# Kernel tuning notes

Hardware: AMD Instinct MI355X
Metric: run time of the kernel (lower is better)

The kernel has to match this reference:

```python
import jax, jax.numpy as jnp
import numpy as np

N = 50000
E = 400000
IN_DIM = 128
HID = 128
OUT = 128
HEADS = 8
NEG_SLOPE = 0.2  # PyG GATConv default
BN_EPS = 1e-5


def _gat_conv(x, W, a_src, a_dst, b, src, dst, concat):
    """PyG GATConv (eval): self-loops added by caller. x:[N,F], W:[F,H*C], a_*:[H,C]."""
    H, C = a_src.shape
    xW = (x @ W).reshape(N, H, C)                       # [N,H,C]
    es = jnp.sum(xW * a_src[None], axis=-1)             # [N,H]
    ed = jnp.sum(xW * a_dst[None], axis=-1)             # [N,H]
    e = jax.nn.leaky_relu(es[src] + ed[dst], NEG_SLOPE) # [E,H]
    m = jax.ops.segment_max(e, dst, num_segments=N)     # softmax over incoming edges per dst
    ex = jnp.exp(e - m[dst])
    denom = jax.ops.segment_sum(ex, dst, num_segments=N)
    alpha = ex / denom[dst]                             # [E,H]
    out = jax.ops.segment_sum(xW[src] * alpha[:, :, None], dst, num_segments=N)  # [N,H,C]
    out = out.reshape(N, H * C) if concat else out.mean(axis=1)
    return out + b


def _bn_eval(h, g, be, rm, rv):
    return (h - rm) * jax.lax.rsqrt(rv + BN_EPS) * g + be


def setup_inputs() -> dict:
    key = jax.random.key(0)
    ks = jax.random.split(key, 20)
    C1 = HID // HEADS
    f32 = jnp.float32
    inp = {
        "x": jax.random.normal(ks[0], (N, IN_DIM), dtype=f32),
        "edge_index": jax.random.randint(ks[1], (2, E), 0, N, dtype=jnp.int64),
        # GAT layer 1 (in->hid, 8 heads, concat)
        "W1": jax.random.normal(ks[2], (IN_DIM, HEADS * C1), dtype=f32) * 0.05,
        "a_src1": jax.random.normal(ks[3], (HEADS, C1), dtype=f32) * 0.05,
        "a_dst1": jax.random.normal(ks[4], (HEADS, C1), dtype=f32) * 0.05,
        "b1": jnp.zeros((HEADS * C1,), dtype=f32),
        # GAT layer 2 (hid->hid, 8 heads, concat)
        "W2": jax.random.normal(ks[5], (HID, HEADS * C1), dtype=f32) * 0.05,
        "a_src2": jax.random.normal(ks[6], (HEADS, C1), dtype=f32) * 0.05,
        "a_dst2": jax.random.normal(ks[7], (HEADS, C1), dtype=f32) * 0.05,
        "b2": jnp.zeros((HEADS * C1,), dtype=f32),
        # GAT layer 3 (hid->out, 1 head, no concat)
        "W3": jax.random.normal(ks[8], (HID, OUT), dtype=f32) * 0.05,
        "a_src3": jax.random.normal(ks[9], (1, OUT), dtype=f32) * 0.05,
        "a_dst3": jax.random.normal(ks[10], (1, OUT), dtype=f32) * 0.05,
        "b3": jnp.zeros((OUT,), dtype=f32),
        # residual linears
        "R1w": jax.random.normal(ks[11], (IN_DIM, HID), dtype=f32) * 0.05,
        "R1b": jnp.zeros((HID,), dtype=f32),
        "R2w": jax.random.normal(ks[12], (HID, HID), dtype=f32) * 0.05,
        "R2b": jnp.zeros((HID,), dtype=f32),
        "R3w": jax.random.normal(ks[13], (HID, OUT), dtype=f32) * 0.05,
        "R3b": jnp.zeros((OUT,), dtype=f32),
        # batch norms (eval mode: running stats)
        "g1": jnp.ones((HID,), dtype=f32), "be1": jnp.zeros((HID,), dtype=f32),
        "rm1": jnp.zeros((HID,), dtype=f32), "rv1": jnp.ones((HID,), dtype=f32),
        "g2": jnp.ones((HID,), dtype=f32), "be2": jnp.zeros((HID,), dtype=f32),
        "rm2": jnp.zeros((HID,), dtype=f32), "rv2": jnp.ones((HID,), dtype=f32),
    }
    return inp


def reference(x, edge_index, W1, a_src1, a_dst1, b1, W2, a_src2, a_dst2, b2,
              W3, a_src3, a_dst3, b3, R1w, R1b, R2w, R2b, R3w, R3b,
              g1, be1, rm1, rv1, g2, be2, rm2, rv2):
    # PyG GATConv adds self-loops by default
    loops = jnp.arange(N, dtype=edge_index.dtype)
    src = jnp.concatenate([edge_index[0], loops])
    dst = jnp.concatenate([edge_index[1], loops])

    h = _gat_conv(x, W1, a_src1, a_dst1, b1, src, dst, concat=True) + (x @ R1w + R1b)
    h1 = jax.nn.relu(_bn_eval(h, g1, be1, rm1, rv1))  # dropout identity in eval

    h = _gat_conv(h1, W2, a_src2, a_dst2, b2, src, dst, concat=True) + (h1 @ R2w + R2b)
    h2 = jax.nn.relu(_bn_eval(h, g2, be2, rm2, rv2))

    out = _gat_conv(h2, W3, a_src3, a_dst3, b3, src, dst, concat=False) + (h2 @ R3w + R3b)
    return out
```

## Files before the change

### kernel.cpp

```cpp
#include <hip/hip_runtime.h>
#include <hip/hip_bf16.h>
#include <type_traits>

typedef __hip_bfloat16 bf16;
typedef __hip_bfloat162 bf162;
typedef short v8s __attribute__((ext_vector_type(8)));
typedef float v4f __attribute__((ext_vector_type(4)));

__device__ __forceinline__ float lrelu(float x) { return x > 0.f ? x : 0.2f * x; }
__device__ __forceinline__ float b2f(bf16 v) { return __bfloat162float(v); }

__global__ void k_count(const int* __restrict__ ei, int* __restrict__ cnt, int E) {
    int i = blockIdx.x * 256 + threadIdx.x;
    if (i < E) atomicAdd(&cnt[ei[E + i]], 1);
}

__global__ void k_scan1(const int* __restrict__ cnt, int* __restrict__ ofs,
                        int* __restrict__ bsum, int n) {
    __shared__ int sh[256];
    int t = threadIdx.x;
    int base = blockIdx.x * 1024 + t * 4;
    int v[4]; int s = 0;
#pragma unroll
    for (int i = 0; i < 4; ++i) { v[i] = (base + i < n) ? cnt[base + i] : 0; s += v[i]; }
    sh[t] = s; __syncthreads();
    for (int o = 1; o < 256; o <<= 1) {
        int x = 0; if (t >= o) x = sh[t - o];
        __syncthreads();
        sh[t] += x;
        __syncthreads();
    }
    int excl = sh[t] - s;
#pragma unroll
    for (int i = 0; i < 4; ++i) { if (base + i < n) ofs[base + i] = excl; excl += v[i]; }
    if (t == 255) bsum[blockIdx.x] = sh[255];
}

__global__ void k_scan2(const int* __restrict__ bsum, int* __restrict__ bpre, int nb) {
    int l = threadIdx.x;
    int v = (l < nb) ? bsum[l] : 0;
    int orig = v;
    for (int o = 1; o < 64; o <<= 1) {
        int x = __shfl_up(v, o);
        if (l >= o) v += x;
    }
    if (l < nb) bpre[l] = v - orig;
}

__global__ void k_scan3(int* __restrict__ ofs, int* __restrict__ cur,
                        const int* __restrict__ bpre, int n) {
    int i = blockIdx.x * 256 + threadIdx.x;
    if (i < n) { int v = ofs[i] + bpre[i >> 10]; ofs[i] = v; cur[i] = v; }
}

__global__ void k_fill(const int* __restrict__ ei, int* __restrict__ cur,
                       int* __restrict__ csr, int E) {
    int i = blockIdx.x * 256 + threadIdx.x;
    if (i < E) {
        int d = ei[E + i];
        int pos = atomicAdd(&cur[d], 1);
        csr[pos] = ei[i];
    }
}

__global__ void k_trans(const float* __restrict__ s0, const float* __restrict__ s1,
                        const float* __restrict__ s2, const float* __restrict__ s3,
                        const float* __restrict__ s4, const float* __restrict__ s5,
                        const float* __restrict__ as1, const float* __restrict__ ad1,
                        const float* __restrict__ as2, const float* __restrict__ ad2,
                        const float* __restrict__ as3, const float* __restrict__ ad3,
                        const float* b1, const float* R1b, const float* g1, const float* be1,
                        const float* rm1, const float* rv1,
                        const float* b2, const float* R2b, const float* g2, const float* be2,
                        const float* rm2, const float* rv2,
                        const float* b3, const float* R3b,
                        bf16* __restrict__ wt, float* __restrict__ prm) {
    int b = blockIdx.x;
    int t = threadIdx.x;
    if (b == 6) {
        int c = t;
        if (c < 128) {
            float s1v = g1[c] * rsqrtf(rv1[c] + 1e-5f);
            prm[c]       = b1[c] + R1b[c];
            prm[128 + c] = s1v;
            prm[256 + c] = be1[c] - rm1[c] * s1v;
            float s2v = g2[c] * rsqrtf(rv2[c] + 1e-5f);
            prm[384 + c] = b2[c] + R2b[c];
            prm[512 + c] = s2v;
            prm[640 + c] = be2[c] - rm2[c] * s2v;
            prm[768 + c] = b3[c] + R3b[c];
        }
        return;
    }
    const float* src;
    switch (b) {
        case 0: src = s0; break; case 1: src = s1; break; case 2: src = s2; break;
        case 3: src = s3; break; case 4: src = s4; break; default: src = s5; break;
    }
    bf16* dst = wt + (size_t)b * 18432;
    for (int i = t; i < 16384; i += 256) {
        int k = i >> 7, n = i & 127;
        dst[n * 128 + k] = __float2bfloat16(src[i]);
    }
    if ((b & 1) == 0) {
        int layer = b >> 1;
        if (layer < 2) {
            const float* asr = (layer == 0) ? as1 : as2;
            const float* ads = (layer == 0) ? ad1 : ad2;
            for (int i = t; i < 2048; i += 256) {
                int row = i >> 7, k = i & 127, h = row & 7;
                const float* av = (row < 8) ? asr : ads;
                float s = 0.f;
#pragma unroll
                for (int c = 0; c < 16; ++c) s += src[k * 128 + h * 16 + c] * av[h * 16 + c];
                dst[(128 + row) * 128 + k] = __float2bfloat16(s);
            }
        } else {
            for (int i = t; i < 2048; i += 256) {
                int row = i >> 7, k = i & 127;
                float s = 0.f;
                if (row == 0 || row == 8) {
                    const float* av = (row == 0) ? as3 : ad3;
                    for (int c = 0; c < 128; ++c) s += src[k * 128 + c] * av[c];
                }
                dst[(128 + row) * 128 + k] = __float2bfloat16(s);
            }
        }
    } else {
        for (int i = t; i < 2048; i += 256)
            dst[16384 + i] = __float2bfloat16(0.f);
    }
}

template <typename T>
__global__ void gemm_dual(const T* __restrict__ A,
                          const bf16* __restrict__ BT0, const bf16* __restrict__ BT1,
                          bf16* __restrict__ O0, bf16* __restrict__ O1,
                          float* __restrict__ es, float* __restrict__ ed,
                          int mode, int nrows) {
    __shared__ bf16 Ash[128 * 128];
    __shared__ bf16 Bsh[144 * 128];
    const bf16* BT = (blockIdx.y == 0) ? BT0 : BT1;
    bf16* O = (blockIdx.y == 0) ? O0 : O1;
    const int t = threadIdx.x;
    const int rowbase = blockIdx.x * 128;
    {
        const int r = t >> 1, hf = t & 1;
        int gr = rowbase + r; if (gr >= nrows) gr = nrows - 1;
        if constexpr (std::is_same<T, float>::value) {
            const float4* asrc = (const float4*)(A + (size_t)gr * 128 + hf * 64);
#pragma unroll
            for (int j = 0; j < 8; ++j) {
                float4 u = asrc[2 * j], w = asrc[2 * j + 1];
                union { bf16 h[8]; float4 f; } tmp;
                tmp.h[0] = __float2bfloat16(u.x); tmp.h[1] = __float2bfloat16(u.y);
                tmp.h[2] = __float2bfloat16(u.z); tmp.h[3] = __float2bfloat16(u.w);
                tmp.h[4] = __float2bfloat16(w.x); tmp.h[5] = __float2bfloat16(w.y);
                tmp.h[6] = __float2bfloat16(w.z); tmp.h[7] = __float2bfloat16(w.w);
                int c = hf * 8 + j, cp = c ^ (r & 7);
                *(float4*)(&Ash[r * 128 + cp * 8]) = tmp.f;
            }
        } else {
            const float4* asrc = (const float4*)(A + (size_t)gr * 128 + hf * 64);
#pragma unroll
            for (int j = 0; j < 8; ++j) {
                int c = hf * 8 + j, cp = c ^ (r & 7);
                *(float4*)(&Ash[r * 128 + cp * 8]) = asrc[j];
            }
        }
    }
    for (int s = t; s < 288; s += 256) {
        int r = s >> 1, hf = s & 1;
        const float4* bsrc = (const float4*)(BT + r * 128 + hf * 64);
#pragma unroll
        for (int j = 0; j < 8; ++j) {
            int c = hf * 8 + j, cp = c ^ (r & 7);
            *(float4*)(&Bsh[r * 128 + cp * 8]) = bsrc[j];
        }
    }
    __syncthreads();
    const int wave = t >> 6, lane = t & 63, quad = lane >> 4, l16 = lane & 15;
    v4f acc[2][9];
#pragma unroll
    for (int i = 0; i < 2; ++i)
#pragma unroll
        for (int j = 0; j < 9; ++j) acc[i][j] = (v4f){0.f, 0.f, 0.f, 0.f};
#pragma unroll
    for (int kit = 0; kit < 4; ++kit) {
        v8s afr[2], bfr[9];
#pragma unroll
        for (int rt = 0; rt < 2; ++rt) {
            int row = wave * 32 + rt * 16 + l16;
            int cp = (kit * 4 + quad) ^ (row & 7);
            afr[rt] = *(const v8s*)(&Ash[row * 128 + cp * 8]);
        }
#pragma unroll
        for (int ct = 0; ct < 9; ++ct) {
            int nn = ct * 16 + l16;
            int cp = (kit * 4 + quad) ^ (nn & 7);
            bfr[ct] = *(const v8s*)(&Bsh[nn * 128 + cp * 8]);
        }
#pragma unroll
        for (int rt = 0; rt < 2; ++rt)
#pragma unroll
            for (int ct = 0; ct < 9; ++ct)
                acc[rt][ct] = __builtin_amdgcn_mfma_f32_16x16x32_bf16(afr[rt], bfr[ct], acc[rt][ct], 0, 0, 0);
    }
#pragma unroll
    for (int rt = 0; rt < 2; ++rt)
#pragma unroll
        for (int ct = 0; ct < 8; ++ct)
#pragma unroll
            for (int r = 0; r < 4; ++r) {
                int gr = rowbase + wave * 32 + rt * 16 + quad * 4 + r;
                if (gr < nrows) O[(size_t)gr * 128 + ct * 16 + l16] = __float2bfloat16(acc[rt][ct][r]);
            }
    if (mode != 0 && blockIdx.y == 0) {
#pragma unroll
        for (int rt = 0; rt < 2; ++rt)
#pragma unroll
            for (int r = 0; r < 4; ++r) {
                int gr = rowbase + wave * 32 + rt * 16 + quad * 4 + r;
                if (gr < nrows) {
                    float v = acc[rt][8][r];
                    if (mode == 1) {
                        if (l16 < 8) es[(size_t)gr * 8 + l16] = v;
                        else         ed[(size_t)gr * 8 + (l16 - 8)] = v;
                    } else {
                        if (l16 == 0) es[gr] = v;
                        else if (l16 == 8) ed[gr] = v;
                    }
                }
            }
    }
}

__global__ void k_agg8(const bf16* __restrict__ xW, const float* __restrict__ es8,
                       const float* __restrict__ ed8,
                       const int* __restrict__ ofs, const int* __restrict__ cur,
                       const int* __restrict__ csr,
                       const bf16* __restrict__ rres, const float* __restrict__ prm,
                       bf16* __restrict__ hout, int n) {
    int wave = threadIdx.x >> 6, lane = threadIdx.x & 63;
    int node = blockIdx.x * 4 + wave;
    if (node >= n) return;
    const int g = lane >> 4, l16 = lane & 15;
    const int c0 = l16 * 8;
    const int hc = l16 >> 1;
    const int he = lane & 7;
    float edw = ed8[(size_t)node * 8 + he];
    float wselfh = __expf(lrelu(es8[(size_t)node * 8 + he] + edw));
    float acc[8]; float den = 0.f;
#pragma unroll
    for (int i = 0; i < 8; ++i) acc[i] = 0.f;
    {
        float ws = __shfl(wselfh, hc);
        if (g == 0) {
            v8s xv = *(const v8s*)(xW + (size_t)node * 128 + c0);
            const bf16* xb = (const bf16*)&xv;
            den = ws;
#pragma unroll
            for (int i = 0; i < 8; ++i) acc[i] = ws * b2f(xb[i]);
        }
    }
    int beg = ofs[node], end = cur[node];
    for (int base = beg; base < end; base += 64) {
        int m = end - base; if (m > 64) m = 64;
        int idx = (lane < m) ? csr[base + lane] : node;
        for (int sub = 0; sub * 8 < m; ++sub) {
            int e = sub * 8 + (lane >> 3);
            int sidx = __shfl(idx, e & 63);
            float esv = es8[(size_t)sidx * 8 + he];
            float w = (e < m) ? __expf(lrelu(esv + edw)) : 0.f;
#pragma unroll
            for (int jj = 0; jj < 2; ++jj) {
                int jo = jj * 4 + g;
                int j = sub * 8 + jo;
                int sv = __shfl(idx, j & 63);
                float wj = __shfl(w, jo * 8 + hc);
                v8s xv = *(const v8s*)(xW + (size_t)sv * 128 + c0);
                const bf16* xb = (const bf16*)&xv;
                den += wj;
#pragma unroll
                for (int i = 0; i < 8; ++i) acc[i] += wj * b2f(xb[i]);
            }
        }
    }
    den += __shfl_xor(den, 16); den += __shfl_xor(den, 32);
#pragma unroll
    for (int i = 0; i < 8; ++i) {
        acc[i] += __shfl_xor(acc[i], 16);
        acc[i] += __shfl_xor(acc[i], 32);
    }
    if (g == 0) {
        float inv = 1.f / den;
        v8s rv = *(const v8s*)(rres + (size_t)node * 128 + c0);
        const bf16* rb = (const bf16*)&rv;
        bf16 outv[8];
#pragma unroll
        for (int i = 0; i < 8; ++i) {
            int c = c0 + i;
            float v = acc[i] * inv + prm[c] + b2f(rb[i]);
            v = fmaxf(v * prm[128 + c] + prm[256 + c], 0.f);
            outv[i] = __float2bfloat16(v);
        }
        *(v8s*)(hout + (size_t)node * 128 + c0) = *(v8s*)outv;
    }
}

__global__ void k_agg1(const bf16* __restrict__ xW, const float* __restrict__ es,
                       const float* __restrict__ ed,
                       const int* __restrict__ ofs, const int* __restrict__ cur,
                       const int* __restrict__ csr,
                       const bf16* __restrict__ rres, const float* __restrict__ bias,
                       float* __restrict__ out, int n) {
    int wave = threadIdx.x >> 6, lane = threadIdx.x & 63;
    int node = blockIdx.x * 4 + wave;
    if (node >= n) return;
    const int g = lane >> 4, l16 = lane & 15;
    const int c0 = l16 * 8;
    float edv = ed[node];
    float wself = __expf(lrelu(es[node] + edv));
    float acc[8]; float den = 0.f;
#pragma unroll
    for (int i = 0; i < 8; ++i) acc[i] = 0.f;
    if (g == 0) {
        v8s xv = *(const v8s*)(xW + (size_t)node * 128 + c0);
        const bf16* xb = (const bf16*)&xv;
        den = wself;
#pragma unroll
        for (int i = 0; i < 8; ++i) acc[i] = wself * b2f(xb[i]);
    }
    int beg = ofs[node], end = cur[node];
    for (int base = beg; base < end; base += 64) {
        int m = end - base; if (m > 64) m = 64;
        int idx = (lane < m) ? csr[base + lane] : node;
        float w = (lane < m) ? __expf(lrelu(es[idx] + edv)) : 0.f;
        for (int j = 0; j < m; j += 4) {
            int jl = j + g;
            int sv = __shfl(idx, jl & 63);
            float wj = __shfl(w, jl & 63);
            if (jl >= m) wj = 0.f;
            v8s xv = *(const v8s*)(xW + (size_t)sv * 128 + c0);
            const bf16* xb = (const bf16*)&xv;
            den += wj;
#pragma unroll
            for (int i = 0; i < 8; ++i) acc[i] += wj * b2f(xb[i]);
        }
    }
    den += __shfl_xor(den, 16); den += __shfl_xor(den, 32);
#pragma unroll
    for (int i = 0; i < 8; ++i) {
        acc[i] += __shfl_xor(acc[i], 16);
        acc[i] += __shfl_xor(acc[i], 32);
    }
    if (g == 0) {
        float inv = 1.f / den;
        v8s rv = *(const v8s*)(rres + (size_t)node * 128 + c0);
        const bf16* rb = (const bf16*)&rv;
        float ov[8];
#pragma unroll
        for (int i = 0; i < 8; ++i)
            ov[i] = acc[i] * inv + bias[c0 + i] + b2f(rb[i]);
        float4 o0, o1;
        o0.x = ov[0]; o0.y = ov[1]; o0.z = ov[2]; o0.w = ov[3];
        o1.x = ov[4]; o1.y = ov[5]; o1.z = ov[6]; o1.w = ov[7];
        *(float4*)(out + (size_t)node * 128 + c0) = o0;
        *(float4*)(out + (size_t)node * 128 + c0 + 4) = o1;
    }
}

extern "C" void kernel_launch(void* const* d_in, const int* in_sizes, int n_in,
                              void* d_out, int out_size, void* d_ws, size_t ws_size,
                              hipStream_t stream) {
    const float* x   = (const float*)d_in[0];
    const int*   ei  = (const int*)d_in[1];
    const float* W1  = (const float*)d_in[2];
    const float* as1 = (const float*)d_in[3];
    const float* ad1 = (const float*)d_in[4];
    const float* b1  = (const float*)d_in[5];
    const float* W2  = (const float*)d_in[6];
    const float* as2 = (const float*)d_in[7];
    const float* ad2 = (const float*)d_in[8];
    const float* b2  = (const float*)d_in[9];
    const float* W3  = (const float*)d_in[10];
    const float* as3 = (const float*)d_in[11];
    const float* ad3 = (const float*)d_in[12];
    const float* b3  = (const float*)d_in[13];
    const float* R1w = (const float*)d_in[14];
    const float* R1b = (const float*)d_in[15];
    const float* R2w = (const float*)d_in[16];
    const float* R2b = (const float*)d_in[17];
    const float* R3w = (const float*)d_in[18];
    const float* R3b = (const float*)d_in[19];
    const float* g1  = (const float*)d_in[20];
    const float* be1 = (const float*)d_in[21];
    const float* rm1 = (const float*)d_in[22];
    const float* rv1 = (const float*)d_in[23];
    const float* g2  = (const float*)d_in[24];
    const float* be2 = (const float*)d_in[25];
    const float* rm2 = (const float*)d_in[26];
    const float* rv2 = (const float*)d_in[27];

    const int N = in_sizes[0] / 128;
    const int E = in_sizes[1] / 2;

    char* p = (char*)d_ws;
    size_t off = 0;
    auto alloc = [&](size_t b) { void* r = p + off; off = (off + b + 255) & ~(size_t)255; return r; };
    int*   cnt  = (int*)alloc((size_t)N * 4);
    int*   ofs  = (int*)alloc((size_t)N * 4);
    int*   cur  = (int*)alloc((size_t)N * 4);
    int*   bsum = (int*)alloc(64 * 4);
    int*   bpre = (int*)alloc(64 * 4);
    int*   csr  = (int*)alloc((size_t)E * 4);
    bf16*  WT   = (bf16*)alloc((size_t)6 * 18432 * 2);
    float* prm  = (float*)alloc(896 * 4);
    float* es   = (float*)alloc((size_t)N * 8 * 4);
    float* ed   = (float*)alloc((size_t)N * 8 * 4);
    bf16*  xW   = (bf16*)alloc((size_t)N * 128 * 2);
    bf16*  rres = (bf16*)alloc((size_t)N * 128 * 2);
    bf16*  hA   = (bf16*)alloc((size_t)N * 128 * 2);
    bf16*  hB   = (bf16*)alloc((size_t)N * 128 * 2);
    (void)ws_size; (void)n_in; (void)out_size;

    hipMemsetAsync(cnt, 0, (size_t)N * 4, stream);
    const int eb = (E + 255) / 256;
    const int nb = (N + 1023) / 1024;
    k_count<<<eb, 256, 0, stream>>>(ei, cnt, E);
    k_scan1<<<nb, 256, 0, stream>>>(cnt, ofs, bsum, N);
    k_scan2<<<1, 64, 0, stream>>>(bsum, bpre, nb);
    k_scan3<<<(N + 255) / 256, 256, 0, stream>>>(ofs, cur, bpre, N);
    k_fill<<<eb, 256, 0, stream>>>(ei, cur, csr, E);
    k_trans<<<7, 256, 0, stream>>>(W1, R1w, W2, R2w, W3, R3w,
                                   as1, ad1, as2, ad2, as3, ad3,
                                   b1, R1b, g1, be1, rm1, rv1,
                                   b2, R2b, g2, be2, rm2, rv2, b3, R3b,
                                   WT, prm);

    const int gx = (N + 127) / 128;
    const int nw = (N + 3) / 4;
    gemm_dual<float><<<dim3(gx, 2), 256, 0, stream>>>(x, WT, WT + 18432, xW, rres, es, ed, 1, N);
    k_agg8<<<nw, 256, 0, stream>>>(xW, es, ed, ofs, cur, csr, rres, prm, hA, N);
    gemm_dual<bf16><<<dim3(gx, 2), 256, 0, stream>>>(hA, WT + 2 * 18432, WT + 3 * 18432, xW, rres, es, ed, 1, N);
    k_agg8<<<nw, 256, 0, stream>>>(xW, es, ed, ofs, cur, csr, rres, prm + 384, hB, N);
    gemm_dual<bf16><<<dim3(gx, 2), 256, 0, stream>>>(hB, WT + 4 * 18432, WT + 5 * 18432, xW, rres, es, ed, 2, N);
    k_agg1<<<nw, 256, 0, stream>>>(xW, es, ed, ofs, cur, csr, rres, prm + 768, (float*)d_out, N);
}
```

Baseline: 346.7 us.

## Fuse all stages into one cooperative persistent kernel with grid syncs

Replaces the dozen separate launches (count, scan, fill, weight transpose, three GEMMs, three aggregations) with a single cooperative kernel of 512 persistent blocks. The stages are separated by grid.sync() and each stage walks its work in grid-stride loops. The GEMM tile shrinks from 128 to 64 rows per job, and the scan is reworked to a per-block reduce plus a single-block prefix. This aims to remove launch and inter-kernel gaps, at the cost of grid-wide barriers, a fixed grid size that may underuse the GPU in heavy phases, and lower per-block GEMM reuse.

```diff
diff --git a/kernel.cpp b/kernel.cpp
--- a/kernel.cpp
+++ b/kernel.cpp
@@ -1,6 +1,8 @@
 #include <hip/hip_runtime.h>
 #include <hip/hip_bf16.h>
-#include <type_traits>
+#include <hip/hip_cooperative_groups.h>
+
+namespace cg = cooperative_groups;
 
 typedef __hip_bfloat16 bf16;
 typedef __hip_bfloat162 bf162;
@@ -10,219 +12,111 @@
 __device__ __forceinline__ float lrelu(float x) { return x > 0.f ? x : 0.2f * x; }
 __device__ __forceinline__ float b2f(bf16 v) { return __bfloat162float(v); }
 
-__global__ void k_count(const int* __restrict__ ei, int* __restrict__ cnt, int E) {
-    int i = blockIdx.x * 256 + threadIdx.x;
-    if (i < E) atomicAdd(&cnt[ei[E + i]], 1);
-}
-
-__global__ void k_scan1(const int* __restrict__ cnt, int* __restrict__ ofs,
-                        int* __restrict__ bsum, int n) {
-    __shared__ int sh[256];
-    int t = threadIdx.x;
-    int base = blockIdx.x * 1024 + t * 4;
-    int v[4]; int s = 0;
-#pragma unroll
-    for (int i = 0; i < 4; ++i) { v[i] = (base + i < n) ? cnt[base + i] : 0; s += v[i]; }
-    sh[t] = s; __syncthreads();
-    for (int o = 1; o < 256; o <<= 1) {
-        int x = 0; if (t >= o) x = sh[t - o];
-        __syncthreads();
-        sh[t] += x;
-        __syncthreads();
-    }
-    int excl = sh[t] - s;
-#pragma unroll
-    for (int i = 0; i < 4; ++i) { if (base + i < n) ofs[base + i] = excl; excl += v[i]; }
-    if (t == 255) bsum[blockIdx.x] = sh[255];
-}
-
-__global__ void k_scan2(const int* __restrict__ bsum, int* __restrict__ bpre, int nb) {
-    int l = threadIdx.x;
-    int v = (l < nb) ? bsum[l] : 0;
-    int orig = v;
-    for (int o = 1; o < 64; o <<= 1) {
-        int x = __shfl_up(v, o);
-        if (l >= o) v += x;
-    }
-    if (l < nb) bpre[l] = v - orig;
-}
-
-__global__ void k_scan3(int* __restrict__ ofs, int* __restrict__ cur,
-                        const int* __restrict__ bpre, int n) {
-    int i = blockIdx.x * 256 + threadIdx.x;
-    if (i < n) { int v = ofs[i] + bpre[i >> 10]; ofs[i] = v; cur[i] = v; }
-}
-
-__global__ void k_fill(const int* __restrict__ ei, int* __restrict__ cur,
-                       int* __restrict__ csr, int E) {
-    int i = blockIdx.x * 256 + threadIdx.x;
-    if (i < E) {
-        int d = ei[E + i];
-        int pos = atomicAdd(&cur[d], 1);
-        csr[pos] = ei[i];
-    }
-}
-
-__global__ void k_trans(const float* __restrict__ s0, const float* __restrict__ s1,
-                        const float* __restrict__ s2, const float* __restrict__ s3,
-                        const float* __restrict__ s4, const float* __restrict__ s5,
-                        const float* __restrict__ as1, const float* __restrict__ ad1,
-                        const float* __restrict__ as2, const float* __restrict__ ad2,
-                        const float* __restrict__ as3, const float* __restrict__ ad3,
-                        const float* b1, const float* R1b, const float* g1, const float* be1,
-                        const float* rm1, const float* rv1,
-                        const float* b2, const float* R2b, const float* g2, const float* be2,
-                        const float* rm2, const float* rv2,
-                        const float* b3, const float* R3b,
-                        bf16* __restrict__ wt, float* __restrict__ prm) {
-    int b = blockIdx.x;
-    int t = threadIdx.x;
-    if (b == 6) {
-        int c = t;
-        if (c < 128) {
-            float s1v = g1[c] * rsqrtf(rv1[c] + 1e-5f);
-            prm[c]       = b1[c] + R1b[c];
-            prm[128 + c] = s1v;
-            prm[256 + c] = be1[c] - rm1[c] * s1v;
-            float s2v = g2[c] * rsqrtf(rv2[c] + 1e-5f);
-            prm[384 + c] = b2[c] + R2b[c];
-            prm[512 + c] = s2v;
-            prm[640 + c] = be2[c] - rm2[c] * s2v;
-            prm[768 + c] = b3[c] + R3b[c];
-        }
-        return;
-    }
-    const float* src;
-    switch (b) {
-        case 0: src = s0; break; case 1: src = s1; break; case 2: src = s2; break;
-        case 3: src = s3; break; case 4: src = s4; break; default: src = s5; break;
-    }
-    bf16* dst = wt + (size_t)b * 18432;
-    for (int i = t; i < 16384; i += 256) {
-        int k = i >> 7, n = i & 127;
-        dst[n * 128 + k] = __float2bfloat16(src[i]);
-    }
-    if ((b & 1) == 0) {
-        int layer = b >> 1;
-        if (layer < 2) {
-            const float* asr = (layer == 0) ? as1 : as2;
-            const float* ads = (layer == 0) ? ad1 : ad2;
-            for (int i = t; i < 2048; i += 256) {
-                int row = i >> 7, k = i & 127, h = row & 7;
-                const float* av = (row < 8) ? asr : ads;
-                float s = 0.f;
-#pragma unroll
-                for (int c = 0; c < 16; ++c) s += src[k * 128 + h * 16 + c] * av[h * 16 + c];
-                dst[(128 + row) * 128 + k] = __float2bfloat16(s);
-            }
-        } else {
-            for (int i = t; i < 2048; i += 256) {
-                int row = i >> 7, k = i & 127;
-                float s = 0.f;
-                if (row == 0 || row == 8) {
-                    const float* av = (row == 0) ? as3 : ad3;
-                    for (int c = 0; c < 128; ++c) s += src[k * 128 + c] * av[c];
-                }
-                dst[(128 + row) * 128 + k] = __float2bfloat16(s);
-            }
-        }
-    } else {
-        for (int i = t; i < 2048; i += 256)
-            dst[16384 + i] = __float2bfloat16(0.f);
-    }
-}
+struct Args {
+    const float* x; const int* ei;
+    const float *W1, *as1, *ad1, *b1;
+    const float *W2, *as2, *ad2, *b2;
+    const float *W3, *as3, *ad3, *b3;
+    const float *R1w, *R1b, *R2w, *R2b, *R3w, *R3b;
+    const float *g1, *be1, *rm1, *rv1, *g2, *be2, *rm2, *rv2;
+    int N, E;
+    int *cnt, *ofs, *cur, *bsum, *bpre, *csr;
+    bf16* WT; float* prm; float *es, *ed;
+    bf16 *xW, *rres, *hA, *hB;
+    float* out;
+};
+
+#define G 512
+#define NT 256
 
 template <typename T>
-__global__ void gemm_dual(const T* __restrict__ A,
-                          const bf16* __restrict__ BT0, const bf16* __restrict__ BT1,
-                          bf16* __restrict__ O0, bf16* __restrict__ O1,
-                          float* __restrict__ es, float* __restrict__ ed,
-                          int mode, int nrows) {
-    __shared__ bf16 Ash[128 * 128];
-    __shared__ bf16 Bsh[144 * 128];
-    const bf16* BT = (blockIdx.y == 0) ? BT0 : BT1;
-    bf16* O = (blockIdx.y == 0) ? O0 : O1;
+__device__ void gemm_phase(const T* __restrict__ A,
+                           const bf16* __restrict__ BT0, const bf16* __restrict__ BT1,
+                           bf16* __restrict__ O0, bf16* __restrict__ O1,
+                           float* __restrict__ es, float* __restrict__ ed,
+                           int mode, int n, char* smem) {
+    bf16* Ash = (bf16*)smem;
+    bf16* Bsh = (bf16*)(smem + 16384);
     const int t = threadIdx.x;
-    const int rowbase = blockIdx.x * 128;
-    {
-        const int r = t >> 1, hf = t & 1;
-        int gr = rowbase + r; if (gr >= nrows) gr = nrows - 1;
-        if constexpr (std::is_same<T, float>::value) {
-            const float4* asrc = (const float4*)(A + (size_t)gr * 128 + hf * 64);
-#pragma unroll
-            for (int j = 0; j < 8; ++j) {
-                float4 u = asrc[2 * j], w = asrc[2 * j + 1];
-                union { bf16 h[8]; float4 f; } tmp;
-                tmp.h[0] = __float2bfloat16(u.x); tmp.h[1] = __float2bfloat16(u.y);
-                tmp.h[2] = __float2bfloat16(u.z); tmp.h[3] = __float2bfloat16(u.w);
-                tmp.h[4] = __float2bfloat16(w.x); tmp.h[5] = __float2bfloat16(w.y);
-                tmp.h[6] = __float2bfloat16(w.z); tmp.h[7] = __float2bfloat16(w.w);
-                int c = hf * 8 + j, cp = c ^ (r & 7);
-                *(float4*)(&Ash[r * 128 + cp * 8]) = tmp.f;
-            }
-        } else {
-            const float4* asrc = (const float4*)(A + (size_t)gr * 128 + hf * 64);
+    const int ntiles = (n + 63) >> 6;
+    const int njobs = ntiles * 2;
+    for (int job = blockIdx.x; job < njobs; job += G) {
+        const int y = (job >= ntiles) ? 1 : 0;
+        const int tile = y ? job - ntiles : job;
+        const bf16* BT = y ? BT1 : BT0;
+        bf16* O = y ? O1 : O0;
+        const int rowbase = tile << 6;
+        {
+            const int r = t >> 2, q = t & 3;
+            int gr = rowbase + r; if (gr >= n) gr = n - 1;
+            if constexpr (__is_same(T, float)) {
+                const float4* asrc = (const float4*)(A + (size_t)gr * 128);
+#pragma unroll
+                for (int j = 0; j < 4; ++j) {
+                    int c = q * 4 + j;
+                    float4 u = asrc[2 * c], w = asrc[2 * c + 1];
+                    union { bf16 h[8]; float4 f; } tmp;
+                    tmp.h[0] = __float2bfloat16(u.x); tmp.h[1] = __float2bfloat16(u.y);
+                    tmp.h[2] = __float2bfloat16(u.z); tmp.h[3] = __float2bfloat16(u.w);
+                    tmp.h[4] = __float2bfloat16(w.x); tmp.h[5] = __float2bfloat16(w.y);
+                    tmp.h[6] = __float2bfloat16(w.z); tmp.h[7] = __float2bfloat16(w.w);
+                    int cp = c ^ (r & 7);
+                    *(float4*)(&Ash[r * 128 + cp * 8]) = tmp.f;
+                }
+            } else {
+                const float4* asrc = (const float4*)(A + (size_t)gr * 128);
+#pragma unroll
+                for (int j = 0; j < 4; ++j) {
+                    int c = q * 4 + j, cp = c ^ (r & 7);
+                    *(float4*)(&Ash[r * 128 + cp * 8]) = asrc[c];
+                }
+            }
+        }
+        for (int s = t; s < 288; s += NT) {
+            int r = s >> 1, hf = s & 1;
+            const float4* bsrc = (const float4*)(BT + r * 128 + hf * 64);
 #pragma unroll
             for (int j = 0; j < 8; ++j) {
                 int c = hf * 8 + j, cp = c ^ (r & 7);
-                *(float4*)(&Ash[r * 128 + cp * 8]) = asrc[j];
-            }
-        }
-    }
-    for (int s = t; s < 288; s += 256) {
-        int r = s >> 1, hf = s & 1;
-        const float4* bsrc = (const float4*)(BT + r * 128 + hf * 64);
-#pragma unroll
-        for (int j = 0; j < 8; ++j) {
-            int c = hf * 8 + j, cp = c ^ (r & 7);
-            *(float4*)(&Bsh[r * 128 + cp * 8]) = bsrc[j];
-        }
-    }
-    __syncthreads();
-    const int wave = t >> 6, lane = t & 63, quad = lane >> 4, l16 = lane & 15;
-    v4f acc[2][9];
-#pragma unroll
-    for (int i = 0; i < 2; ++i)
-#pragma unroll
-        for (int j = 0; j < 9; ++j) acc[i][j] = (v4f){0.f, 0.f, 0.f, 0.f};
-#pragma unroll
-    for (int kit = 0; kit < 4; ++kit) {
-        v8s afr[2], bfr[9];
-#pragma unroll
-        for (int rt = 0; rt < 2; ++rt) {
-            int row = wave * 32 + rt * 16 + l16;
-            int cp = (kit * 4 + quad) ^ (row & 7);
-            afr[rt] = *(const v8s*)(&Ash[row * 128 + cp * 8]);
-        }
-#pragma unroll
-        for (int ct = 0; ct < 9; ++ct) {
-            int nn = ct * 16 + l16;
-            int cp = (kit * 4 + quad) ^ (nn & 7);
-            bfr[ct] = *(const v8s*)(&Bsh[nn * 128 + cp * 8]);
-        }
-#pragma unroll
-        for (int rt = 0; rt < 2; ++rt)
+                *(float4*)(&Bsh[r * 128 + cp * 8]) = bsrc[j];
+            }
+        }
+        __syncthreads();
+        const int wave = t >> 6, lane = t & 63, quad = lane >> 4, l16 = lane & 15;
+        v4f acc[9];
+#pragma unroll
+        for (int j = 0; j < 9; ++j) acc[j] = (v4f){0.f, 0.f, 0.f, 0.f};
+#pragma unroll
+        for (int kit = 0; kit < 4; ++kit) {
+            v8s afr, bfr[9];
+            {
+                int row = wave * 16 + l16;
+                int cp = (kit * 4 + quad) ^ (row & 7);
+                afr = *(const v8s*)(&Ash[row * 128 + cp * 8]);
+            }
+#pragma unroll
+            for (int ct = 0; ct < 9; ++ct) {
+                int nn = ct * 16 + l16;
+                int cp = (kit * 4 + quad) ^ (nn & 7);
+                bfr[ct] = *(const v8s*)(&Bsh[nn * 128 + cp * 8]);
+            }
 #pragma unroll
             for (int ct = 0; ct < 9; ++ct)
-                acc[rt][ct] = __builtin_amdgcn_mfma_f32_16x16x32_bf16(afr[rt], bfr[ct], acc[rt][ct], 0, 0, 0);
-    }
-#pragma unroll
-    for (int rt = 0; rt < 2; ++rt)
+                acc[ct] = __builtin_amdgcn_mfma_f32_16x16x32_bf16(afr, bfr[ct], acc[ct], 0, 0, 0);
+        }
 #pragma unroll
         for (int ct = 0; ct < 8; ++ct)
 #pragma unroll
             for (int r = 0; r < 4; ++r) {
-                int gr = rowbase + wave * 32 + rt * 16 + quad * 4 + r;
-                if (gr < nrows) O[(size_t)gr * 128 + ct * 16 + l16] = __float2bfloat16(acc[rt][ct][r]);
-            }
-    if (mode != 0 && blockIdx.y == 0) {
-#pragma unroll
-        for (int rt = 0; rt < 2; ++rt)
+                int gr = rowbase + wave * 16 + quad * 4 + r;
+                if (gr < n) O[(size_t)gr * 128 + ct * 16 + l16] = __float2bfloat16(acc[ct][r]);
+            }
+        if (mode != 0 && y == 0) {
 #pragma unroll
             for (int r = 0; r < 4; ++r) {
-                int gr = rowbase + wave * 32 + rt * 16 + quad * 4 + r;
-                if (gr < nrows) {
-                    float v = acc[rt][8][r];
+                int gr = rowbase + wave * 16 + quad * 4 + r;
+                if (gr < n) {
+                    float v = acc[8][r];
                     if (mode == 1) {
                         if (l16 < 8) es[(size_t)gr * 8 + l16] = v;
                         else         ed[(size_t)gr * 8 + (l16 - 8)] = v;
@@ -232,218 +126,337 @@
                     }
                 }
             }
+        }
+        __syncthreads();
     }
 }
 
-__global__ void k_agg8(const bf16* __restrict__ xW, const float* __restrict__ es8,
-                       const float* __restrict__ ed8,
-                       const int* __restrict__ ofs, const int* __restrict__ cur,
-                       const int* __restrict__ csr,
-                       const bf16* __restrict__ rres, const float* __restrict__ prm,
-                       bf16* __restrict__ hout, int n) {
-    int wave = threadIdx.x >> 6, lane = threadIdx.x & 63;
-    int node = blockIdx.x * 4 + wave;
-    if (node >= n) return;
+__device__ void agg8_phase(const bf16* __restrict__ xW, const float* __restrict__ es8,
+                           const float* __restrict__ ed8,
+                           const int* __restrict__ ofs, const int* __restrict__ cur,
+                           const int* __restrict__ csr,
+                           const bf16* __restrict__ rres, const float* __restrict__ prm,
+                           bf16* __restrict__ hout, int n) {
+    const int wave = threadIdx.x >> 6, lane = threadIdx.x & 63;
+    const int g = lane >> 4, l16 = lane & 15;
+    const int c0 = l16 * 8, hc = l16 >> 1, he = lane & 7;
+    const int nw = (n + 3) >> 2;
+    for (int job = blockIdx.x; job < nw; job += G) {
+        int node = job * 4 + wave;
+        if (node < n) {
+            float edw = ed8[(size_t)node * 8 + he];
+            float wselfh = __expf(lrelu(es8[(size_t)node * 8 + he] + edw));
+            float acc[8]; float den = 0.f;
+#pragma unroll
+            for (int i = 0; i < 8; ++i) acc[i] = 0.f;
+            {
+                float ws = __shfl(wselfh, hc);
+                if (g == 0) {
+                    v8s xv = *(const v8s*)(xW + (size_t)node * 128 + c0);
+                    const bf16* xb = (const bf16*)&xv;
+                    den = ws;
+#pragma unroll
+                    for (int i = 0; i < 8; ++i) acc[i] = ws * b2f(xb[i]);
+                }
+            }
+            int beg = ofs[node], end = cur[node];
+            for (int base = beg; base < end; base += 64) {
+                int m = end - base; if (m > 64) m = 64;
+                int idx = (lane < m) ? csr[base + lane] : node;
+                for (int sub = 0; sub * 8 < m; ++sub) {
+                    int e = sub * 8 + (lane >> 3);
+                    int sidx = __shfl(idx, e & 63);
+                    float esv = es8[(size_t)sidx * 8 + he];
+                    float w = (e < m) ? __expf(lrelu(esv + edw)) : 0.f;
+#pragma unroll
+                    for (int jj = 0; jj < 2; ++jj) {
+                        int jo = jj * 4 + g;
+                        int j = sub * 8 + jo;
+                        int sv = __shfl(idx, j & 63);
+                        float wj = __shfl(w, jo * 8 + hc);
+                        v8s xv = *(const v8s*)(xW + (size_t)sv * 128 + c0);
+                        const bf16* xb = (const bf16*)&xv;
+                        den += wj;
+#pragma unroll
+                        for (int i = 0; i < 8; ++i) acc[i] += wj * b2f(xb[i]);
+                    }
+                }
+            }
+            den += __shfl_xor(den, 16); den += __shfl_xor(den, 32);
+#pragma unroll
+            for (int i = 0; i < 8; ++i) {
+                acc[i] += __shfl_xor(acc[i], 16);
+                acc[i] += __shfl_xor(acc[i], 32);
+            }
+            if (g == 0) {
+                float inv = 1.f / den;
+                v8s rv = *(const v8s*)(rres + (size_t)node * 128 + c0);
+                const bf16* rb = (const bf16*)&rv;
+                bf16 outv[8];
+#pragma unroll
+                for (int i = 0; i < 8; ++i) {
+                    int c = c0 + i;
+                    float v = acc[i] * inv + prm[c] + b2f(rb[i]);
+                    v = fmaxf(v * prm[128 + c] + prm[256 + c], 0.f);
+                    outv[i] = __float2bfloat16(v);
+                }
+                *(v8s*)(hout + (size_t)node * 128 + c0) = *(v8s*)outv;
+            }
+        }
+    }
+}
+
+__device__ void agg1_phase(const bf16* __restrict__ xW, const float* __restrict__ es,
+                           const float* __restrict__ ed,
+                           const int* __restrict__ ofs, const int* __restrict__ cur,
+                           const int* __restrict__ csr,
+                           const bf16* __restrict__ rres, const float* __restrict__ bias,
+                           float* __restrict__ out, int n) {
+    const int wave = threadIdx.x >> 6, lane = threadIdx.x & 63;
     const int g = lane >> 4, l16 = lane & 15;
     const int c0 = l16 * 8;
-    const int hc = l16 >> 1;
-    const int he = lane & 7;
-    float edw = ed8[(size_t)node * 8 + he];
-    float wselfh = __expf(lrelu(es8[(size_t)node * 8 + he] + edw));
-    float acc[8]; float den = 0.f;
-#pragma unroll
-    for (int i = 0; i < 8; ++i) acc[i] = 0.f;
+    const int nw = (n + 3) >> 2;
+    for (int job = blockIdx.x; job < nw; job += G) {
+        int node = job * 4 + wave;
+        if (node < n) {
+            float edv = ed[node];
+            float wself = __expf(lrelu(es[node] + edv));
+            float acc[8]; float den = 0.f;
+#pragma unroll
+            for (int i = 0; i < 8; ++i) acc[i] = 0.f;
+            if (g == 0) {
+                v8s xv = *(const v8s*)(xW + (size_t)node * 128 + c0);
+                const bf16* xb = (const bf16*)&xv;
+                den = wself;
+#pragma unroll
+                for (int i = 0; i < 8; ++i) acc[i] = wself * b2f(xb[i]);
+            }
+            int beg = ofs[node], end = cur[node];
+            for (int base = beg; base < end; base += 64) {
+                int m = end - base; if (m > 64) m = 64;
+                int idx = (lane < m) ? csr[base + lane] : node;
+                float w = (lane < m) ? __expf(lrelu(es[idx] + edv)) : 0.f;
+                for (int j = 0; j < m; j += 4) {
+                    int jl = j + g;
+                    int sv = __shfl(idx, jl & 63);
+                    float wj = __shfl(w, jl & 63);
+                    if (jl >= m) wj = 0.f;
+                    v8s xv = *(const v8s*)(xW + (size_t)sv * 128 + c0);
+                    const bf16* xb = (const bf16*)&xv;
+                    den += wj;
+#pragma unroll
+                    for (int i = 0; i < 8; ++i) acc[i] += wj * b2f(xb[i]);
+                }
+            }
+            den += __shfl_xor(den, 16); den += __shfl_xor(den, 32);
+#pragma unroll
+            for (int i = 0; i < 8; ++i) {
+                acc[i] += __shfl_xor(acc[i], 16);
+                acc[i] += __shfl_xor(acc[i], 32);
+            }
+            if (g == 0) {
+                float inv = 1.f / den;
+                v8s rv = *(const v8s*)(rres + (size_t)node * 128 + c0);
+                const bf16* rb = (const bf16*)&rv;
+                float ov[8];
+#pragma unroll
+                for (int i = 0; i < 8; ++i)
+                    ov[i] = acc[i] * inv + bias[c0 + i] + b2f(rb[i]);
+                float4 o0, o1;
+                o0.x = ov[0]; o0.y = ov[1]; o0.z = ov[2]; o0.w = ov[3];
+                o1.x = ov[4]; o1.y = ov[5]; o1.z = ov[6]; o1.w = ov[7];
+                *(float4*)(out + (size_t)node * 128 + c0) = o0;
+                *(float4*)(out + (size_t)node * 128 + c0 + 4) = o1;
+            }
+        }
+    }
+}
+
+__global__ __launch_bounds__(NT, 2) void mega(Args a) {
+    __shared__ alignas(16) char smem[53248];
+    int* ish = (int*)smem;
+    cg::grid_group grid = cg::this_grid();
+    const int t = threadIdx.x;
+    const int b = blockIdx.x;
+    const int N = a.N, E = a.E;
+    const int C = (N + G - 1) / G;
+
+    for (int i = b * NT + t; i < N; i += G * NT) a.cnt[i] = 0;
+    if (b < 6) {
+        const float* src;
+        switch (b) {
+            case 0: src = a.W1; break; case 1: src = a.R1w; break; case 2: src = a.W2; break;
+            case 3: src = a.R2w; break; case 4: src = a.W3; break; default: src = a.R3w; break;
+        }
+        bf16* dst = a.WT + (size_t)b * 18432;
+        for (int i = t; i < 16384; i += NT) {
+            int k = i >> 7, n = i & 127;
+            dst[n * 128 + k] = __float2bfloat16(src[i]);
+        }
+        if ((b & 1) == 0) {
+            int layer = b >> 1;
+            if (layer < 2) {
+                const float* asr = (layer == 0) ? a.as1 : a.as2;
+                const float* ads = (layer == 0) ? a.ad1 : a.ad2;
+                for (int i = t; i < 2048; i += NT) {
+                    int row = i >> 7, k = i & 127, h = row & 7;
+                    const float* av = (row < 8) ? asr : ads;
+                    float s = 0.f;
+#pragma unroll
+                    for (int c = 0; c < 16; ++c) s += src[k * 128 + h * 16 + c] * av[h * 16 + c];
+                    dst[(128 + row) * 128 + k] = __float2bfloat16(s);
+                }
+            } else {
+                for (int i = t; i < 2048; i += NT) {
+                    int row = i >> 7, k = i & 127;
+                    float s = 0.f;
+                    if (row == 0 || row == 8) {
+                        const float* av = (row == 0) ? a.as3 : a.ad3;
+                        for (int c = 0; c < 128; ++c) s += src[k * 128 + c] * av[c];
+                    }
+                    dst[(128 + row) * 128 + k] = __float2bfloat16(s);
+                }
+            }
+        } else {
+            for (int i = t; i < 2048; i += NT)
+                dst[16384 + i] = __float2bfloat16(0.f);
+        }
+    } else if (b == 6 && t < 128) {
+        int c = t;
+        float s1v = a.g1[c] * rsqrtf(a.rv1[c] + 1e-5f);
+        a.prm[c]       = a.b1[c] + a.R1b[c];
+        a.prm[128 + c] = s1v;
+        a.prm[256 + c] = a.be1[c] - a.rm1[c] * s1v;
+        float s2v = a.g2[c] * rsqrtf(a.rv2[c] + 1e-5f);
+        a.prm[384 + c] = a.b2[c] + a.R2b[c];
+        a.prm[512 + c] = s2v;
+        a.prm[640 + c] = a.be2[c] - a.rm2[c] * s2v;
+        a.prm[768 + c] = a.b3[c] + a.R3b[c];
+    }
+    grid.sync();
+
+    for (int i = b * NT + t; i < E; i += G * NT)
+        atomicAdd(&a.cnt[a.ei[E + i]], 1);
+    grid.sync();
+
     {
-        float ws = __shfl(wselfh, hc);
-        if (g == 0) {
-            v8s xv = *(const v8s*)(xW + (size_t)node * 128 + c0);
-            const bf16* xb = (const bf16*)&xv;
-            den = ws;
-#pragma unroll
-            for (int i = 0; i < 8; ++i) acc[i] = ws * b2f(xb[i]);
-        }
-    }
-    int beg = ofs[node], end = cur[node];
-    for (int base = beg; base < end; base += 64) {
-        int m = end - base; if (m > 64) m = 64;
-        int idx = (lane < m) ? csr[base + lane] : node;
-        for (int sub = 0; sub * 8 < m; ++sub) {
-            int e = sub * 8 + (lane >> 3);
-            int sidx = __shfl(idx, e & 63);
-            float esv = es8[(size_t)sidx * 8 + he];
-            float w = (e < m) ? __expf(lrelu(esv + edw)) : 0.f;
-#pragma unroll
-            for (int jj = 0; jj < 2; ++jj) {
-                int jo = jj * 4 + g;
-                int j = sub * 8 + jo;
-                int sv = __shfl(idx, j & 63);
-                float wj = __shfl(w, jo * 8 + hc);
-                v8s xv = *(const v8s*)(xW + (size_t)sv * 128 + c0);
-                const bf16* xb = (const bf16*)&xv;
-                den += wj;
-#pragma unroll
-                for (int i = 0; i < 8; ++i) acc[i] += wj * b2f(xb[i]);
-            }
-        }
-    }
-    den += __shfl_xor(den, 16); den += __shfl_xor(den, 32);
-#pragma unroll
-    for (int i = 0; i < 8; ++i) {
-        acc[i] += __shfl_xor(acc[i], 16);
-        acc[i] += __shfl_xor(acc[i], 32);
-    }
-    if (g == 0) {
-        float inv = 1.f / den;
-        v8s rv = *(const v8s*)(rres + (size_t)node * 128 + c0);
-        const bf16* rb = (const bf16*)&rv;
-        bf16 outv[8];
-#pragma unroll
-        for (int i = 0; i < 8; ++i) {
-            int c = c0 + i;
-            float v = acc[i] * inv + prm[c] + b2f(rb[i]);
-            v = fmaxf(v * prm[128 + c] + prm[256 + c], 0.f);
-            outv[i] = __float2bfloat16(v);
-        }
-        *(v8s*)(hout + (size_t)node * 128 + c0) = *(v8s*)outv;
-    }
-}
-
-__global__ void k_agg1(const bf16* __restrict__ xW, const float* __restrict__ es,
-                       const float* __restrict__ ed,
-                       const int* __restrict__ ofs, const int* __restrict__ cur,
-                       const int* __restrict__ csr,
-                       const bf16* __restrict__ rres, const float* __restrict__ bias,
-                       float* __restrict__ out, int n) {
-    int wave = threadIdx.x >> 6, lane = threadIdx.x & 63;
-    int node = blockIdx.x * 4 + wave;
-    if (node >= n) return;
-    const int g = lane >> 4, l16 = lane & 15;
-    const int c0 = l16 * 8;
-    float edv = ed[node];
-    float wself = __expf(lrelu(es[node] + edv));
-    float acc[8]; float den = 0.f;
-#pragma unroll
-    for (int i = 0; i < 8; ++i) acc[i] = 0.f;
-    if (g == 0) {
-        v8s xv = *(const v8s*)(xW + (size_t)node * 128 + c0);
-        const bf16* xb = (const bf16*)&xv;
-        den = wself;
-#pragma unroll
-        for (int i = 0; i < 8; ++i) acc[i] = wself * b2f(xb[i]);
-    }
-    int beg = ofs[node], end = cur[node];
-    for (int base = beg; base < end; base += 64) {
-        int m = end - base; if (m > 64) m = 64;
-        int idx = (lane < m) ? csr[base + lane] : node;
-        float w = (lane < m) ? __expf(lrelu(es[idx] + edv)) : 0.f;
-        for (int j = 0; j < m; j += 4) {
-            int jl = j + g;
-            int sv = __shfl(idx, jl & 63);
-            float wj = __shfl(w, jl & 63);
-            if (jl >= m) wj = 0.f;
-            v8s xv = *(const v8s*)(xW + (size_t)sv * 128 + c0);
-            const bf16* xb = (const bf16*)&xv;
-            den += wj;
-#pragma unroll
-            for (int i = 0; i < 8; ++i) acc[i] += wj * b2f(xb[i]);
-        }
-    }
-    den += __shfl_xor(den, 16); den += __shfl_xor(den, 32);
-#pragma unroll
-    for (int i = 0; i < 8; ++i) {
-        acc[i] += __shfl_xor(acc[i], 16);
-        acc[i] += __shfl_xor(acc[i], 32);
-    }
-    if (g == 0) {
-        float inv = 1.f / den;
-        v8s rv = *(const v8s*)(rres + (size_t)node * 128 + c0);
-        const bf16* rb = (const bf16*)&rv;
-        float ov[8];
-#pragma unroll
-        for (int i = 0; i < 8; ++i)
-            ov[i] = acc[i] * inv + bias[c0 + i] + b2f(rb[i]);
-        float4 o0, o1;
-        o0.x = ov[0]; o0.y = ov[1]; o0.z = ov[2]; o0.w = ov[3];
-        o1.x = ov[4]; o1.y = ov[5]; o1.z = ov[6]; o1.w = ov[7];
-        *(float4*)(out + (size_t)node * 128 + c0) = o0;
-        *(float4*)(out + (size_t)node * 128 + c0 + 4) = o1;
-    }
+        int i = b * C + t;
+        int v = (t < C && i < N) ? a.cnt[i] : 0;
+        ish[t] = v; __syncthreads();
+        for (int o = 128; o > 0; o >>= 1) {
+            if (t < o) ish[t] += ish[t + o];
+            __syncthreads();
+        }
+        if (t == 0) a.bsum[b] = ish[0];
+    }
+    grid.sync();
+
+    if (b == 0) {
+        int s0 = a.bsum[2 * t], s1 = a.bsum[2 * t + 1];
+        int p = s0 + s1;
+        ish[t] = p; __syncthreads();
+        for (int o = 1; o < 256; o <<= 1) {
+            int x = 0; if (t >= o) x = ish[t - o];
+            __syncthreads();
+            ish[t] += x;
+            __syncthreads();
+        }
+        int excl = ish[t] - p;
+        a.bpre[2 * t] = excl;
+        a.bpre[2 * t + 1] = excl + s0;
+    }
+    grid.sync();
+
+    {
+        int i = b * C + t;
+        int v = (t < C && i < N) ? a.cnt[i] : 0;
+        ish[t] = v; __syncthreads();
+        for (int o = 1; o < 256; o <<= 1) {
+            int x = 0; if (t >= o) x = ish[t - o];
+            __syncthreads();
+            ish[t] += x;
+            __syncthreads();
+        }
+        int excl = ish[t] - v + a.bpre[b];
+        if (t < C && i < N) { a.ofs[i] = excl; a.cur[i] = excl; }
+    }
+    grid.sync();
+
+    for (int i = b * NT + t; i < E; i += G * NT) {
+        int d = a.ei[E + i];
+        int pos = atomicAdd(&a.cur[d], 1);
+        a.csr[pos] = a.ei[i];
+    }
+    grid.sync();
+
+    gemm_phase<float>(a.x, a.WT, a.WT + 18432, a.xW, a.rres, a.es, a.ed, 1, N, smem);
+    grid.sync();
+    agg8_phase(a.xW, a.es, a.ed, a.ofs, a.cur, a.csr, a.rres, a.prm, a.hA, N);
+    grid.sync();
+    gemm_phase<bf16>(a.hA, a.WT + 2 * 18432, a.WT + 3 * 18432, a.xW, a.rres, a.es, a.ed, 1, N, smem);
+    grid.sync();
+    agg8_phase(a.xW, a.es, a.ed, a.ofs, a.cur, a.csr, a.rres, a.prm + 384, a.hB, N);
+    grid.sync();
+    gemm_phase<bf16>(a.hB, a.WT + 4 * 18432, a.WT + 5 * 18432, a.xW, a.rres, a.es, a.ed, 2, N, smem);
+    grid.sync();
+    agg1_phase(a.xW, a.es, a.ed, a.ofs, a.cur, a.csr, a.rres, a.prm + 768, a.out, N);
 }
 
 extern "C" void kernel_launch(void* const* d_in, const int* in_sizes, int n_in,
                               void* d_out, int out_size, void* d_ws, size_t ws_size,
                               hipStream_t stream) {
-    const float* x   = (const float*)d_in[0];
-    const int*   ei  = (const int*)d_in[1];
-    const float* W1  = (const float*)d_in[2];
-    const float* as1 = (const float*)d_in[3];
-    const float* ad1 = (const float*)d_in[4];
-    const float* b1  = (const float*)d_in[5];
-    const float* W2  = (const float*)d_in[6];
-    const float* as2 = (const float*)d_in[7];
-    const float* ad2 = (const float*)d_in[8];
-    const float* b2  = (const float*)d_in[9];
-    const float* W3  = (const float*)d_in[10];
-    const float* as3 = (const float*)d_in[11];
-    const float* ad3 = (const float*)d_in[12];
-    const float* b3  = (const float*)d_in[13];
-    const float* R1w = (const float*)d_in[14];
-    const float* R1b = (const float*)d_in[15];
-    const float* R2w = (const float*)d_in[16];
-    const float* R2b = (const float*)d_in[17];
-    const float* R3w = (const float*)d_in[18];
-    const float* R3b = (const float*)d_in[19];
-    const float* g1  = (const float*)d_in[20];
-    const float* be1 = (const float*)d_in[21];
-    const float* rm1 = (const float*)d_in[22];
-    const float* rv1 = (const float*)d_in[23];
-    const float* g2  = (const float*)d_in[24];
-    const float* be2 = (const float*)d_in[25];
-    const float* rm2 = (const float*)d_in[26];
-    const float* rv2 = (const float*)d_in[27];
-
-    const int N = in_sizes[0] / 128;
-    const int E = in_sizes[1] / 2;
+    Args a;
+    a.x   = (const float*)d_in[0];
+    a.ei  = (const int*)d_in[1];
+    a.W1  = (const float*)d_in[2];
+    a.as1 = (const float*)d_in[3];
+    a.ad1 = (const float*)d_in[4];
+    a.b1  = (const float*)d_in[5];
+    a.W2  = (const float*)d_in[6];
+    a.as2 = (const float*)d_in[7];
+    a.ad2 = (const float*)d_in[8];
+    a.b2  = (const float*)d_in[9];
+    a.W3  = (const float*)d_in[10];
+    a.as3 = (const float*)d_in[11];
+    a.ad3 = (const float*)d_in[12];
+    a.b3  = (const float*)d_in[13];
+    a.R1w = (const float*)d_in[14];
+    a.R1b = (const float*)d_in[15];
+    a.R2w = (const float*)d_in[16];
+    a.R2b = (const float*)d_in[17];
+    a.R3w = (const float*)d_in[18];
+    a.R3b = (const float*)d_in[19];
+    a.g1  = (const float*)d_in[20];
+    a.be1 = (const float*)d_in[21];
+    a.rm1 = (const float*)d_in[22];
+    a.rv1 = (const float*)d_in[23];
+    a.g2  = (const float*)d_in[24];
+    a.be2 = (const float*)d_in[25];
+    a.rm2 = (const float*)d_in[26];
+    a.rv2 = (const float*)d_in[27];
+    a.N = in_sizes[0] / 128;
+    a.E = in_sizes[1] / 2;
 
     char* p = (char*)d_ws;
     size_t off = 0;
-    auto alloc = [&](size_t b) { void* r = p + off; off = (off + b + 255) & ~(size_t)255; return r; };
-    int*   cnt  = (int*)alloc((size_t)N * 4);
-    int*   ofs  = (int*)alloc((size_t)N * 4);
-    int*   cur  = (int*)alloc((size_t)N * 4);
-    int*   bsum = (int*)alloc(64 * 4);
-    int*   bpre = (int*)alloc(64 * 4);
-    int*   csr  = (int*)alloc((size_t)E * 4);
-    bf16*  WT   = (bf16*)alloc((size_t)6 * 18432 * 2);
-    float* prm  = (float*)alloc(896 * 4);
-    float* es   = (float*)alloc((size_t)N * 8 * 4);
-    float* ed   = (float*)alloc((size_t)N * 8 * 4);
-    bf16*  xW   = (bf16*)alloc((size_t)N * 128 * 2);
-    bf16*  rres = (bf16*)alloc((size_t)N * 128 * 2);
-    bf16*  hA   = (bf16*)alloc((size_t)N * 128 * 2);
-    bf16*  hB   = (bf16*)alloc((size_t)N * 128 * 2);
+    auto alloc = [&](size_t bytes) { void* r = p + off; off = (off + bytes + 255) & ~(size_t)255; return r; };
+    a.cnt  = (int*)alloc((size_t)a.N * 4);
+    a.ofs  = (int*)alloc((size_t)a.N * 4);
+    a.cur  = (int*)alloc((size_t)a.N * 4);
+    a.bsum = (int*)alloc(G * 4);
+    a.bpre = (int*)alloc(G * 4);
+    a.csr  = (int*)alloc((size_t)a.E * 4);
+    a.WT   = (bf16*)alloc((size_t)6 * 18432 * 2);
+    a.prm  = (float*)alloc(896 * 4);
+    a.es   = (float*)alloc((size_t)a.N * 8 * 4);
+    a.ed   = (float*)alloc((size_t)a.N * 8 * 4);
+    a.xW   = (bf16*)alloc((size_t)a.N * 128 * 2);
+    a.rres = (bf16*)alloc((size_t)a.N * 128 * 2);
+    a.hA   = (bf16*)alloc((size_t)a.N * 128 * 2);
+    a.hB   = (bf16*)alloc((size_t)a.N * 128 * 2);
+    a.out  = (float*)d_out;
     (void)ws_size; (void)n_in; (void)out_size;
 
-    hipMemsetAsync(cnt, 0, (size_t)N * 4, stream);
-    const int eb = (E + 255) / 256;
-    const int nb = (N + 1023) / 1024;
-    k_count<<<eb, 256, 0, stream>>>(ei, cnt, E);
-    k_scan1<<<nb, 256, 0, stream>>>(cnt, ofs, bsum, N);
-    k_scan2<<<1, 64, 0, stream>>>(bsum, bpre, nb);
-    k_scan3<<<(N + 255) / 256, 256, 0, stream>>>(ofs, cur, bpre, N);
-    k_fill<<<eb, 256, 0, stream>>>(ei, cur, csr, E);
-    k_trans<<<7, 256, 0, stream>>>(W1, R1w, W2, R2w, W3, R3w,
-                                   as1, ad1, as2, ad2, as3, ad3,
-                                   b1, R1b, g1, be1, rm1, rv1,
-                                   b2, R2b, g2, be2, rm2, rv2, b3, R3b,
-                                   WT, prm);
-
-    const int gx = (N + 127) / 128;
-    const int nw = (N + 3) / 4;
-    gemm_dual<float><<<dim3(gx, 2), 256, 0, stream>>>(x, WT, WT + 18432, xW, rres, es, ed, 1, N);
-    k_agg8<<<nw, 256, 0, stream>>>(xW, es, ed, ofs, cur, csr, rres, prm, hA, N);
-    gemm_dual<bf16><<<dim3(gx, 2), 256, 0, stream>>>(hA, WT + 2 * 18432, WT + 3 * 18432, xW, rres, es, ed, 1, N);
-    k_agg8<<<nw, 256, 0, stream>>>(xW, es, ed, ofs, cur, csr, rres, prm + 384, hB, N);
-    gemm_dual<bf16><<<dim3(gx, 2), 256, 0, stream>>>(hB, WT + 4 * 18432, WT + 5 * 18432, xW, rres, es, ed, 2, N);
-    k_agg1<<<nw, 256, 0, stream>>>(xW, es, ed, ofs, cur, csr, rres, prm + 768, (float*)d_out, N);
+    void* params[] = { &a };
+    hipLaunchCooperativeKernel((const void*)mega, dim3(G), dim3(NT), params, 0, stream);
 }
```

After: 1.115 ms. +221.7%, slower.
